# Kernel optimization log

Measured on AMD Instinct MI355X. Metric: run time of the kernel, lower is better.

Reference implementation:

```python
import jax, jax.numpy as jnp
import numpy as np

NODE_CARDS = [119, 5, 12, 12, 10, 6, 6, 2, 2]
EDGE_CARDS = [5, 6, 2]
HIDDEN = 256
LAYERS = 5
N = 60000
E = 180000
G = 2048  # num graphs (fixed num_segments)
BN_EPS = 1e-5

_NODE_OFFS = np.concatenate([[0], np.cumsum(NODE_CARDS[:-1])]).astype(np.int32)
_EDGE_OFFS = np.concatenate([[0], np.cumsum(EDGE_CARDS[:-1])]).astype(np.int32)
_NODE_MAX = np.asarray(NODE_CARDS, np.int32) - 1
_EDGE_MAX = np.asarray(EDGE_CARDS, np.int32) - 1


def _cat_sum(x, table, maxs, offs):
    # x: [N, F] int; table: [sum(cards), H] -> [N, H]
    idx = jnp.clip(x, 0, maxs[None, :]) + offs[None, :]
    return table[idx].sum(axis=1)


def setup_inputs() -> dict:
    key = jax.random.key(0)
    ks = jax.random.split(key, 32)
    w = 0.0625  # ~ xavier for 256

    def nrm(k, shape, s=w):
        return jax.random.normal(k, shape, dtype=jnp.float32) * s

    inp = {
        'x': jax.random.randint(ks[0], (N, len(NODE_CARDS)), 0, 119, dtype=jnp.int32),
        'edge_index': jax.random.randint(ks[1], (2, E), 0, N, dtype=jnp.int32),
        'edge_attr': jax.random.randint(ks[2], (E, len(EDGE_CARDS)), 0, 6, dtype=jnp.int32),
        'batch': jnp.sort(jax.random.randint(ks[3], (N,), 0, G, dtype=jnp.int32)),
        # embeddings
        'node_emb': nrm(ks[4], (int(sum(NODE_CARDS)), HIDDEN), 0.1),
        'edge_emb': nrm(ks[5], (int(sum(EDGE_CARDS)), HIDDEN), 0.1),
        'vn_emb': nrm(ks[6], (1, HIDDEN), 0.1),
        # GINE conv: eps + 2-layer MLP per layer (stacked)
        'eps': jnp.zeros((LAYERS,), jnp.float32),
        'W1': nrm(ks[7], (LAYERS, HIDDEN, HIDDEN)),
        'b1': jnp.zeros((LAYERS, HIDDEN), jnp.float32),
        'W2': nrm(ks[8], (LAYERS, HIDDEN, HIDDEN)),
        'b2': jnp.zeros((LAYERS, HIDDEN), jnp.float32),
        # BatchNorm (eval mode: running stats)
        'bn_gamma': jnp.ones((LAYERS, HIDDEN), jnp.float32),
        'bn_beta': jnp.zeros((LAYERS, HIDDEN), jnp.float32),
        'bn_mean': nrm(ks[9], (LAYERS, HIDDEN), 0.02),
        'bn_var': jnp.ones((LAYERS, HIDDEN), jnp.float32),
        # virtual-node MLP per layer
        'vW1': nrm(ks[10], (LAYERS, HIDDEN, HIDDEN)),
        'vb1': jnp.zeros((LAYERS, HIDDEN), jnp.float32),
        'vW2': nrm(ks[11], (LAYERS, HIDDEN, HIDDEN)),
        'vb2': jnp.zeros((LAYERS, HIDDEN), jnp.float32),
        # head MLP (2 layers: hidden->hidden->1)
        'hW1': nrm(ks[12], (HIDDEN, HIDDEN)),
        'hb1': jnp.zeros((HIDDEN,), jnp.float32),
        'hW2': nrm(ks[13], (HIDDEN, 1)),
        'hb2': jnp.zeros((1,), jnp.float32),
    }
    return inp


def reference(x, edge_index, edge_attr, batch,
              node_emb, edge_emb, vn_emb, eps,
              W1, b1, W2, b2,
              bn_gamma, bn_beta, bn_mean, bn_var,
              vW1, vb1, vW2, vb2,
              hW1, hb1, hW2, hb2):
    node_maxs = jnp.asarray(_NODE_MAX)
    node_offs = jnp.asarray(_NODE_OFFS)
    edge_maxs = jnp.asarray(_EDGE_MAX)
    edge_offs = jnp.asarray(_EDGE_OFFS)

    h = _cat_sum(x, node_emb, node_maxs, node_offs)          # [N, H]
    ea = _cat_sum(edge_attr, edge_emb, edge_maxs, edge_offs)  # [E, H]
    src, dst = edge_index[0], edge_index[1]

    vn = jnp.broadcast_to(vn_emb[0], (G, HIDDEN))  # [G, H]

    def mean_pool(h_):
        s = jax.ops.segment_sum(h_, batch, num_segments=G)
        cnt = jax.ops.segment_sum(jnp.ones((h_.shape[0], 1), h_.dtype), batch, num_segments=G)
        return s / jnp.maximum(cnt, 1.0)

    for l in range(LAYERS):
        h = h + vn[batch]
        # GINEConv: msg = relu(x_src + edge_attr); agg scatter-add onto dst
        msg = jax.nn.relu(h[src] + ea)                        # [E, H]
        agg = jax.ops.segment_sum(msg, dst, num_segments=N)   # [N, H]
        z = (1.0 + eps[l]) * h + agg
        z = jax.nn.relu(z @ W1[l] + b1[l]) @ W2[l] + b2[l]
        # BatchNorm1d (eval, running stats)
        z = (z - bn_mean[l]) * (bn_gamma[l] / jnp.sqrt(bn_var[l] + BN_EPS)) + bn_beta[l]
        h = jax.nn.relu(z)
        # virtual-node update
        g = mean_pool(h)
        vn = vn + (jax.nn.relu(g @ vW1[l] + vb1[l]) @ vW2[l] + vb2[l])

    g = mean_pool(h)                                          # [G, H]
    logits = (jax.nn.relu(g @ hW1 + hb1) @ hW2 + hb2).reshape(-1)  # [G]
    return logits
```

## Files before the change

kernel.cpp:

```cpp
#include <hip/hip_runtime.h>

#define NN 60000
#define NE 180000
#define NG 2048
#define NL 5
#define CAP 32

typedef unsigned short u16;
typedef unsigned int u32;
typedef __bf16 bf16x8 __attribute__((ext_vector_type(8)));
typedef float f32x4 __attribute__((ext_vector_type(4)));

__device__ __forceinline__ u16 f2bf(float f) {
    u32 u = __builtin_bit_cast(u32, f);
    u += 0x7FFFu + ((u >> 16) & 1u);
    return (u16)(u >> 16);
}
__device__ __forceinline__ float bf2f(u16 s) {
    return __builtin_bit_cast(float, (u32)s << 16);
}
__device__ __forceinline__ float bflo(u32 w) {
    return __builtin_bit_cast(float, w << 16);
}
__device__ __forceinline__ float bfhi(u32 w) {
    return __builtin_bit_cast(float, w & 0xFFFF0000u);
}
__device__ __forceinline__ u32 pack2bf(float lo, float hi) {
    return (u32)f2bf(lo) | ((u32)f2bf(hi) << 16);
}
__device__ __forceinline__ void gload_lds16(const void* g, void* l) {
    __builtin_amdgcn_global_load_lds(
        (const __attribute__((address_space(1))) unsigned int*)g,
        (__attribute__((address_space(3))) unsigned int*)l, 16, 0, 0);
}
__device__ __forceinline__ int swz(int row, int col) {
    return (row << 9) + ((((col >> 3) ^ (row & 7))) << 4) + ((col & 7) << 1);
}

__constant__ int NODE_OFF[9]  = {0, 119, 124, 136, 148, 158, 164, 170, 172};
__constant__ int NODE_MAXC[9] = {118, 4, 11, 11, 9, 5, 5, 1, 1};

__global__ __launch_bounds__(256) void k_prep_weights(
    const float* __restrict__ W1, const float* __restrict__ W2,
    const float* __restrict__ vW1, const float* __restrict__ vW2,
    const float* __restrict__ hW1, u16* __restrict__ Wt)
{
    int mat = blockIdx.x >> 8;
    int n = blockIdx.x & 255;
    int k = threadIdx.x;
    const float* src;
    if (mat < 5)       src = W1 + (size_t)mat * 65536;
    else if (mat < 10) src = W2 + (size_t)(mat - 5) * 65536;
    else if (mat < 15) src = vW1 + (size_t)(mat - 10) * 65536;
    else if (mat < 20) src = vW2 + (size_t)(mat - 15) * 65536;
    else               src = hW1;
    Wt[(size_t)mat * 65536 + n * 256 + k] = f2bf(src[k * 256 + n]);
}

__global__ __launch_bounds__(256) void k_misc(
    const float* __restrict__ eemb, const int* __restrict__ batch,
    const float* __restrict__ vn_emb,
    u16* __restrict__ comb, int* __restrict__ starts,
    float* __restrict__ vn, u16* __restrict__ vnbf, float* __restrict__ gsum)
{
    int b = blockIdx.x;
    if (b < 2048) {
        int i = b * 256 + threadIdx.x;
        float v = vn_emb[i & 255];
        vn[i] = v;
        vnbf[i] = f2bf(v);
        gsum[i] = 0.f;
    } else if (b < 2108) {
        int r = b - 2048, c = threadIdx.x;
        int a0 = r / 12, a1 = (r % 12) / 2, a2 = r & 1;
        comb[r * 256 + c] = f2bf(eemb[a0 * 256 + c] + eemb[(5 + a1) * 256 + c] +
                                 eemb[(11 + a2) * 256 + c]);
    } else {
        int g = (b - 2108) * 256 + threadIdx.x;
        if (g > NG) return;
        int lo = 0, hi = NN;
        while (lo < hi) {
            int mid = (lo + hi) >> 1;
            if (batch[mid] < g) lo = mid + 1; else hi = mid;
        }
        starts[g] = lo;
    }
}

__global__ __launch_bounds__(256) void k_embed(const int* __restrict__ x,
                                               const float* __restrict__ node_emb,
                                               u16* __restrict__ hbf,
                                               int* __restrict__ deg)
{
    int i = blockIdx.x * 4 + (threadIdx.x >> 6);
    if (i >= NN) return;
    if ((threadIdx.x & 63) == 0) deg[i] = 0;
    int c = (threadIdx.x & 63) * 4;
    float4 s = make_float4(0.f, 0.f, 0.f, 0.f);
#pragma unroll
    for (int f = 0; f < 9; ++f) {
        int xv = x[i * 9 + f];
        xv = xv < 0 ? 0 : (xv > NODE_MAXC[f] ? NODE_MAXC[f] : xv);
        const float4 t = *(const float4*)&node_emb[(size_t)(NODE_OFF[f] + xv) * 256 + c];
        s.x += t.x; s.y += t.y; s.z += t.z; s.w += t.w;
    }
    ushort4 o;
    o.x = f2bf(s.x); o.y = f2bf(s.y); o.z = f2bf(s.z); o.w = f2bf(s.w);
    *(ushort4*)&hbf[(size_t)i * 256 + c] = o;
}

__global__ __launch_bounds__(256) void k_bucket(
    const int* __restrict__ src, const int* __restrict__ dst,
    const int* __restrict__ eattr, int* __restrict__ deg, u32* __restrict__ slots)
{
    int e = blockIdx.x * 256 + threadIdx.x;
    if (e >= NE) return;
    int a0 = eattr[e * 3 + 0]; a0 = a0 < 0 ? 0 : (a0 > 4 ? 4 : a0);
    int a1 = eattr[e * 3 + 1]; a1 = a1 < 0 ? 0 : (a1 > 5 ? 5 : a1);
    int a2 = eattr[e * 3 + 2]; a2 = a2 < 0 ? 0 : (a2 > 1 ? 1 : a2);
    u32 code = (u32)(a0 * 12 + a1 * 2 + a2);
    int d = dst[e];
    int p = atomicAdd(&deg[d], 1);
    if (p < CAP) slots[(size_t)d * CAP + p] = (u32)src[e] | (code << 17);
}

__global__ __launch_bounds__(256) void k_agg(
    const u16* __restrict__ hbf, const u16* __restrict__ vnbf,
    const int* __restrict__ batch, const u32* __restrict__ slots,
    const int* __restrict__ deg, const u16* __restrict__ comb,
    u16* __restrict__ Abf, const float* __restrict__ epsp)
{
    const int wid = threadIdx.x >> 6, lane = threadIdx.x & 63;
    const int half = lane >> 5, l32 = lane & 31;
    const int d = blockIdx.x * 8 + wid * 2 + half;
    const int c = l32 * 8;
    int nd = deg[d];
    nd = nd > CAP ? CAP : nd;

    const u32* sl = slots + (size_t)d * CAP;
    u32 sv_l = (l32 < nd) ? sl[l32] : 0u;
    int b_l = (l32 < nd) ? batch[sv_l & 0x1FFFFu] : 0;

    float acc[8] = {0.f, 0.f, 0.f, 0.f, 0.f, 0.f, 0.f, 0.f};
    for (int p = 0; p < nd; ++p) {
        int srcl = (lane & 32) | p;
        u32 sv = (u32)__shfl((int)sv_l, srcl);
        int b  = __shfl(b_l, srcl);
        int s  = (int)(sv & 0x1FFFFu);
        int code = (int)(sv >> 17);
        const uint4 hv = *(const uint4*)&hbf[(size_t)s * 256 + c];
        const uint4 vv = *(const uint4*)&vnbf[(size_t)b * 256 + c];
        const uint4 tv = *(const uint4*)&comb[(size_t)code * 256 + c];
        const u32* hw = (const u32*)&hv;
        const u32* vw = (const u32*)&vv;
        const u32* tw = (const u32*)&tv;
#pragma unroll
        for (int e = 0; e < 4; ++e) {
            acc[e * 2 + 0] += fmaxf(bflo(hw[e]) + bflo(vw[e]) + bflo(tw[e]), 0.f);
            acc[e * 2 + 1] += fmaxf(bfhi(hw[e]) + bfhi(vw[e]) + bfhi(tw[e]), 0.f);
        }
    }

    int bd = batch[d];
    float ep = 1.0f + *epsp;
    const uint4 hd = *(const uint4*)&hbf[(size_t)d * 256 + c];
    const uint4 vd = *(const uint4*)&vnbf[(size_t)bd * 256 + c];
    const u32* hw = (const u32*)&hd;
    const u32* vw = (const u32*)&vd;
    uint4 o;
    u32* op = (u32*)&o;
#pragma unroll
    for (int e = 0; e < 4; ++e) {
        float lo = (bflo(hw[e]) + bflo(vw[e])) * ep + acc[e * 2 + 0];
        float hi = (bfhi(hw[e]) + bfhi(vw[e])) * ep + acc[e * 2 + 1];
        op[e] = pack2bf(lo, hi);
    }
    *(uint4*)&Abf[(size_t)d * 256 + c] = o;
}

__global__ __launch_bounds__(512, 2) void k_mlp2(
    const u16* __restrict__ Abf, u16* __restrict__ hnxt,
    const int* __restrict__ batch,
    const u16* __restrict__ W1t, const u16* __restrict__ W2t,
    const float* __restrict__ b1, const float* __restrict__ b2,
    const float* __restrict__ bng, const float* __restrict__ bnb,
    const float* __restrict__ bnm, const float* __restrict__ bnv,
    float* __restrict__ gsum)
{
    __shared__ __align__(16) u16 Tl[128 * 256];
    __shared__ int batchLds[128];
    const int m0 = blockIdx.x * 128;
    const int tid = threadIdx.x, lane = tid & 63, wid = tid >> 6;
    const int wn = wid * 32;
    const int cl = lane & 15, rg = lane >> 4;

    if (tid < 128) batchLds[tid] = (m0 + tid < NN) ? batch[m0 + tid] : -1;

    bf16x8 B1[2][8], B2[2][8];
#pragma unroll
    for (int j = 0; j < 2; ++j) {
        const char* w1p = (const char*)W1t + (size_t)(wn + j * 16 + cl) * 512 + (rg << 4);
        const char* w2p = (const char*)W2t + (size_t)(wn + j * 16 + cl) * 512 + (rg << 4);
#pragma unroll
        for (int ks = 0; ks < 8; ++ks) {
            B1[j][ks] = __builtin_bit_cast(bf16x8, *(const uint4*)(w1p + ks * 64));
            B2[j][ks] = __builtin_bit_cast(bf16x8, *(const uint4*)(w2p + ks * 64));
        }
    }

#pragma unroll
    for (int i = 0; i < 8; ++i) {
        int slot = i * 512 + tid;
        int row = slot >> 5, cch = slot & 31;
        int g = cch ^ (row & 7);
        gload_lds16((const char*)Abf + (size_t)(m0 + row) * 512 + (g << 4),
                    (char*)Tl + ((i * 512 + wid * 64) << 4));
    }
    __syncthreads();

    f32x4 acc[8][2] = {};
#pragma unroll
    for (int ks = 0; ks < 8; ++ks) {
#pragma unroll
        for (int i = 0; i < 8; ++i) {
            int ar = i * 16 + cl;
            int ch = ks * 4 + rg;
            bf16x8 af = __builtin_bit_cast(bf16x8,
                *(const uint4*)((const char*)Tl + (ar << 9) + ((ch ^ (ar & 7)) << 4)));
#pragma unroll
            for (int j = 0; j < 2; ++j)
                acc[i][j] = __builtin_amdgcn_mfma_f32_16x16x32_bf16(af, B1[j][ks], acc[i][j], 0, 0, 0);
        }
    }
    __syncthreads();

#pragma unroll
    for (int j = 0; j < 2; ++j) {
        int col = wn + j * 16 + cl;
        float bv = b1[col];
#pragma unroll
        for (int i = 0; i < 8; ++i)
#pragma unroll
            for (int r = 0; r < 4; ++r) {
                int row = i * 16 + rg * 4 + r;
                float v = fmaxf(acc[i][j][r] + bv, 0.f);
                *(u16*)((char*)Tl + swz(row, col)) = f2bf(v);
            }
    }
    __syncthreads();

#pragma unroll
    for (int i = 0; i < 8; ++i)
#pragma unroll
        for (int j = 0; j < 2; ++j)
            acc[i][j] = f32x4{0.f, 0.f, 0.f, 0.f};
#pragma unroll
    for (int ks = 0; ks < 8; ++ks) {
#pragma unroll
        for (int i = 0; i < 8; ++i) {
            int ar = i * 16 + cl;
            int ch = ks * 4 + rg;
            bf16x8 af = __builtin_bit_cast(bf16x8,
                *(const uint4*)((const char*)Tl + (ar << 9) + ((ch ^ (ar & 7)) << 4)));
#pragma unroll
            for (int j = 0; j < 2; ++j)
                acc[i][j] = __builtin_amdgcn_mfma_f32_16x16x32_bf16(af, B2[j][ks], acc[i][j], 0, 0, 0);
        }
    }

#pragma unroll
    for (int j = 0; j < 2; ++j) {
        int gn = wn + j * 16 + cl;
        float bv = b2[gn];
        float sc = bng[gn] * rsqrtf(bnv[gn] + 1e-5f);
        float sh = bnb[gn] - bnm[gn] * sc;
        float s = 0.f;
        int gcur = -1;
#pragma unroll
        for (int i = 0; i < 8; ++i) {
#pragma unroll
            for (int r = 0; r < 4; ++r) {
                int row = i * 16 + rg * 4 + r;
                int g = batchLds[row];
                float v = acc[i][j][r] + bv;
                u16 hb = f2bf(fmaxf(v * sc + sh, 0.f));
                if (g >= 0) hnxt[(size_t)(m0 + row) * 256 + gn] = hb;
                if (g != gcur) {
                    if (gcur >= 0) atomicAdd(&gsum[(size_t)gcur * 256 + gn], s);
                    gcur = g; s = 0.f;
                }
                if (g >= 0) s += bf2f(hb);
            }
        }
        if (gcur >= 0) atomicAdd(&gsum[(size_t)gcur * 256 + gn], s);
    }
}

__device__ __forceinline__ void stageW(const u16* __restrict__ W, u16* Bl,
                                       int k0, int tid, int wid)
{
#pragma unroll
    for (int i = 0; i < 4; ++i) {
        int slot = i * 512 + tid;
        int row = slot >> 3, cch = slot & 7;
        int g = cch ^ (row & 7);
        gload_lds16((const char*)W + (size_t)row * 512 + (size_t)k0 * 2 + (g << 4),
                    (char*)Bl + ((i * 512 + wid * 64) << 4));
    }
}

__device__ __forceinline__ void gemm64(const u16* Tl, u16* Bl, const u16* __restrict__ W,
                                       f32x4 (&acc)[2][4], int wm, int wn,
                                       int lane, int tid, int wid)
{
    const int cl = lane & 15;
    for (int k0 = 0; k0 < 256; k0 += 64) {
        __syncthreads();
        stageW(W, Bl, k0, tid, wid);
        __syncthreads();
#pragma unroll
        for (int kw = 0; kw < 2; ++kw) {
            int q = kw * 4 + (lane >> 4);
            int qt = (k0 >> 3) + q;
            bf16x8 af[2], bfr[4];
#pragma unroll
            for (int t = 0; t < 2; ++t) {
                int ar = wm + t * 16 + cl;
                af[t] = __builtin_bit_cast(bf16x8,
                    *(const uint4*)((const char*)Tl + (ar << 9) + ((qt ^ (ar & 7)) << 4)));
            }
#pragma unroll
            for (int t = 0; t < 4; ++t) {
                int br = wn + t * 16 + cl;
                bfr[t] = __builtin_bit_cast(bf16x8,
                    *(const uint4*)((const char*)Bl + (br << 7) + ((q ^ (br & 7)) << 4)));
            }
#pragma unroll
            for (int i = 0; i < 2; ++i)
#pragma unroll
                for (int j = 0; j < 4; ++j)
                    acc[i][j] = __builtin_amdgcn_mfma_f32_16x16x32_bf16(af[i], bfr[j], acc[i][j], 0, 0, 0);
        }
    }
}

__device__ __forceinline__ void writeT(u16* Tl, const f32x4 (&acc)[2][4],
                                       const float* __restrict__ b1,
                                       int wm, int wn, int lane)
{
    const int cl = lane & 15, rg = lane >> 4;
#pragma unroll
    for (int j = 0; j < 4; ++j) {
        int col = wn + j * 16 + cl;
        float bv = b1[col];
#pragma unroll
        for (int i = 0; i < 2; ++i)
#pragma unroll
            for (int r = 0; r < 4; ++r) {
                int row = wm + i * 16 + rg * 4 + r;
                float v = fmaxf(acc[i][j][r] + bv, 0.f);
                *(u16*)((char*)Tl + swz(row, col)) = f2bf(v);
            }
    }
}

__global__ __launch_bounds__(512) void k_vnmlp(
    float* __restrict__ gsum, const int* __restrict__ starts,
    const u16* __restrict__ W1t, const u16* __restrict__ W2t,
    const float* __restrict__ b1, const float* __restrict__ b2,
    float* __restrict__ vn, u16* __restrict__ vnbf)
{
    __shared__ __align__(16) u16 Bl[256 * 64];
    __shared__ __align__(16) u16 Tl[64 * 256];
    const int m0 = blockIdx.x * 64;
    const int tid = threadIdx.x, lane = tid & 63, wid = tid >> 6;
    const int wm = (wid >> 2) * 32, wn = (wid & 3) * 64;
    const int cl = lane & 15, rg = lane >> 4;

    {
        const int c = lane * 4;
#pragma unroll
        for (int n = 0; n < 8; ++n) {
            int row = wid * 8 + n;
            int g = m0 + row;
            float4 sv = *(const float4*)&gsum[(size_t)g * 256 + c];
            *(float4*)&gsum[(size_t)g * 256 + c] = make_float4(0.f, 0.f, 0.f, 0.f);
            float cnt = (float)(starts[g + 1] - starts[g]);
            float inv = 1.0f / fmaxf(cnt, 1.0f);
            ushort4 o;
            o.x = f2bf(sv.x * inv); o.y = f2bf(sv.y * inv);
            o.z = f2bf(sv.z * inv); o.w = f2bf(sv.w * inv);
            *(ushort4*)((char*)Tl + swz(row, c)) = o;
        }
    }
    __syncthreads();

    f32x4 acc1[2][4] = {};
    gemm64(Tl, Bl, W1t, acc1, wm, wn, lane, tid, wid);
    __syncthreads();
    writeT(Tl, acc1, b1, wm, wn, lane);

    f32x4 acc2[2][4] = {};
    gemm64(Tl, Bl, W2t, acc2, wm, wn, lane, tid, wid);

#pragma unroll
    for (int j = 0; j < 4; ++j) {
        int gn = wn + j * 16 + cl;
        float bv = b2[gn];
#pragma unroll
        for (int i = 0; i < 2; ++i) {
#pragma unroll
            for (int r = 0; r < 4; ++r) {
                int gm = m0 + wm + i * 16 + rg * 4 + r;
                size_t idx = (size_t)gm * 256 + gn;
                float nv = vn[idx] + acc2[i][j][r] + bv;
                vn[idx] = nv;
                vnbf[idx] = f2bf(nv);
            }
        }
    }
}

__global__ __launch_bounds__(512) void k_headf(
    const float* __restrict__ gsum, const int* __restrict__ starts,
    const u16* __restrict__ W1t, const float* __restrict__ b1,
    const float* __restrict__ hW2, const float* __restrict__ hb2,
    float* __restrict__ out)
{
    __shared__ __align__(16) u16 Bl[256 * 64];
    __shared__ __align__(16) u16 Tl[64 * 256];
    const int m0 = blockIdx.x * 64;
    const int tid = threadIdx.x, lane = tid & 63, wid = tid >> 6;
    const int wm = (wid >> 2) * 32, wn = (wid & 3) * 64;

    {
        const int c = lane * 4;
#pragma unroll
        for (int n = 0; n < 8; ++n) {
            int row = wid * 8 + n;
            int g = m0 + row;
            float4 sv = *(const float4*)&gsum[(size_t)g * 256 + c];
            float cnt = (float)(starts[g + 1] - starts[g]);
            float inv = 1.0f / fmaxf(cnt, 1.0f);
            ushort4 o;
            o.x = f2bf(sv.x * inv); o.y = f2bf(sv.y * inv);
            o.z = f2bf(sv.z * inv); o.w = f2bf(sv.w * inv);
            *(ushort4*)((char*)Tl + swz(row, c)) = o;
        }
    }
    __syncthreads();

    f32x4 acc1[2][4] = {};
    gemm64(Tl, Bl, W1t, acc1, wm, wn, lane, tid, wid);
    __syncthreads();
    writeT(Tl, acc1, b1, wm, wn, lane);
    __syncthreads();

    int row = tid >> 3, oct = tid & 7;
    float s = 0.f;
#pragma unroll
    for (int c = 0; c < 32; ++c) {
        int col = oct * 32 + c;
        s += bf2f(*(const u16*)((const char*)Tl + swz(row, col))) * hW2[col];
    }
    s += __shfl_down(s, 4);
    s += __shfl_down(s, 2);
    s += __shfl_down(s, 1);
    if (oct == 0) out[m0 + row] = s + hb2[0];
}

extern "C" void kernel_launch(void* const* d_in, const int* in_sizes, int n_in,
                              void* d_out, int out_size, void* d_ws, size_t ws_size,
                              hipStream_t stream)
{
    const int*   x        = (const int*)d_in[0];
    const int*   ei       = (const int*)d_in[1];
    const int*   eattr    = (const int*)d_in[2];
    const int*   batch    = (const int*)d_in[3];
    const float* node_emb = (const float*)d_in[4];
    const float* edge_emb = (const float*)d_in[5];
    const float* vn_emb   = (const float*)d_in[6];
    const float* eps      = (const float*)d_in[7];
    const float* W1       = (const float*)d_in[8];
    const float* b1       = (const float*)d_in[9];
    const float* W2       = (const float*)d_in[10];
    const float* b2       = (const float*)d_in[11];
    const float* bng      = (const float*)d_in[12];
    const float* bnb      = (const float*)d_in[13];
    const float* bnm      = (const float*)d_in[14];
    const float* bnv      = (const float*)d_in[15];
    const float* vW1      = (const float*)d_in[16];
    const float* vb1      = (const float*)d_in[17];
    const float* vW2      = (const float*)d_in[18];
    const float* vb2      = (const float*)d_in[19];
    const float* hW1      = (const float*)d_in[20];
    const float* hb1      = (const float*)d_in[21];
    const float* hW2      = (const float*)d_in[22];
    const float* hb2      = (const float*)d_in[23];
    float* out = (float*)d_out;

    char* ws = (char*)d_ws;
    size_t off = 0;
    auto alloc = [&](size_t b) {
        char* p = ws + off;
        off = (off + b + 255) & ~(size_t)255;
        return p;
    };
    u16*   hbf0 = (u16*)alloc((size_t)NN * 256 * 2);
    u16*   hbf1 = (u16*)alloc((size_t)NN * 256 * 2);
    u16*   Abf  = (u16*)alloc((size_t)NN * 256 * 2 + 65536);
    float* vn   = (float*)alloc((size_t)NG * 256 * 4);
    u16*   vnbf = (u16*)alloc((size_t)NG * 256 * 2);
    float* gsum = (float*)alloc((size_t)NG * 256 * 4);
    u16*   Wt   = (u16*)alloc((size_t)21 * 65536 * 2);
    int*   starts = (int*)alloc((size_t)(NG + 1) * 4);
    u16*   comb = (u16*)alloc((size_t)60 * 256 * 2);
    int*   deg  = (int*)alloc((size_t)NN * 4);
    u32*   slots = (u32*)alloc((size_t)NN * CAP * 4);

    const int* srcI = ei;
    const int* dstI = ei + NE;

    k_prep_weights<<<21 * 256, 256, 0, stream>>>(W1, W2, vW1, vW2, hW1, Wt);
    k_misc<<<2117, 256, 0, stream>>>(edge_emb, batch, vn_emb, comb, starts, vn, vnbf, gsum);
    k_embed<<<NN / 4, 256, 0, stream>>>(x, node_emb, hbf0, deg);
    k_bucket<<<(NE + 255) / 256, 256, 0, stream>>>(srcI, dstI, eattr, deg, slots);

    const int GBIG = (NN + 127) / 128;
    const int GSM  = NG / 64;

    u16* hcur = hbf0;
    u16* hnxt = hbf1;
    for (int l = 0; l < NL; ++l) {
        k_agg<<<NN / 8, 256, 0, stream>>>(hcur, vnbf, batch, slots, deg, comb, Abf, eps + l);
        k_mlp2<<<GBIG, 512, 0, stream>>>(Abf, hnxt, batch,
                                         Wt + (size_t)(0 + l) * 65536,
                                         Wt + (size_t)(5 + l) * 65536,
                                         b1 + l * 256, b2 + l * 256,
                                         bng + l * 256, bnb + l * 256,
                                         bnm + l * 256, bnv + l * 256,
                                         gsum);
        if (l < NL - 1) {
            k_vnmlp<<<GSM, 512, 0, stream>>>(gsum, starts,
                                             Wt + (size_t)(10 + l) * 65536,
                                             Wt + (size_t)(15 + l) * 65536,
                                             vb1 + l * 256, vb2 + l * 256,
                                             vn, vnbf);
        }
        u16* t = hcur; hcur = hnxt; hnxt = t;
    }
    k_headf<<<GSM, 512, 0, stream>>>(gsum, starts, Wt + (size_t)20 * 65536,
                                     hb1, hW2, hb2, out);
}
```

Measured before the change: 551.8 us.

## Halve MLP row tile and stream weights in K-halves to raise occupancy

The fused two-layer MLP kernel now handles 64 rows per block instead of 128. Weights are loaded in two K-halves that are reused across register buffers, so the next half's weights load while the current half's MFMAs run. Register and LDS use per block roughly halve, which lets launch bounds request 4 blocks per CU instead of 2 and doubles the grid to fill the GPU better. In exchange each block re-reads all weights for half as many rows, doubling global weight traffic per row. The extra blocks also double the atomic flushes of the per-graph pooled sums.

```diff
diff --git a/kernel.cpp b/kernel.cpp
--- a/kernel.cpp
+++ b/kernel.cpp
@@ -178,7 +178,36 @@
     *(uint4*)&Abf[(size_t)d * 256 + c] = o;
 }
 
-__global__ __launch_bounds__(512, 2) void k_mlp2(
+__device__ __forceinline__ void loadW(bf16x8 (&B)[2][4], const u16* __restrict__ W,
+                                      int hk, int wn, int cl, int rg)
+{
+#pragma unroll
+    for (int j = 0; j < 2; ++j) {
+        const char* p = (const char*)W + (size_t)(wn + j * 16 + cl) * 512 + hk * 256 + (rg << 4);
+#pragma unroll
+        for (int ks = 0; ks < 4; ++ks)
+            B[j][ks] = __builtin_bit_cast(bf16x8, *(const uint4*)(p + ks * 64));
+    }
+}
+
+__device__ __forceinline__ void gemmHalf(f32x4 (&acc)[4][2], const bf16x8 (&B)[2][4],
+                                         const u16* Tl, int hk, int cl, int rg)
+{
+#pragma unroll
+    for (int ks = 0; ks < 4; ++ks) {
+#pragma unroll
+        for (int i = 0; i < 4; ++i) {
+            int ar = i * 16 + cl;
+            int ch = hk * 16 + ks * 4 + rg;
+            bf16x8 af = __builtin_bit_cast(bf16x8,
+                *(const uint4*)((const char*)Tl + (ar << 9) + ((ch ^ (ar & 7)) << 4)));
+            acc[i][0] = __builtin_amdgcn_mfma_f32_16x16x32_bf16(af, B[0][ks], acc[i][0], 0, 0, 0);
+            acc[i][1] = __builtin_amdgcn_mfma_f32_16x16x32_bf16(af, B[1][ks], acc[i][1], 0, 0, 0);
+        }
+    }
+}
+
+__global__ __launch_bounds__(512, 4) void k_mlp3(
     const u16* __restrict__ Abf, u16* __restrict__ hnxt,
     const int* __restrict__ batch,
     const u16* __restrict__ W1t, const u16* __restrict__ W2t,
@@ -187,51 +216,35 @@
     const float* __restrict__ bnm, const float* __restrict__ bnv,
     float* __restrict__ gsum)
 {
-    __shared__ __align__(16) u16 Tl[128 * 256];
-    __shared__ int batchLds[128];
-    const int m0 = blockIdx.x * 128;
+    __shared__ __align__(16) u16 Tl[64 * 256];
+    __shared__ int batchLds[64];
+    const int m0 = blockIdx.x * 64;
     const int tid = threadIdx.x, lane = tid & 63, wid = tid >> 6;
     const int wn = wid * 32;
     const int cl = lane & 15, rg = lane >> 4;
 
-    if (tid < 128) batchLds[tid] = (m0 + tid < NN) ? batch[m0 + tid] : -1;
-
-    bf16x8 B1[2][8], B2[2][8];
-#pragma unroll
-    for (int j = 0; j < 2; ++j) {
-        const char* w1p = (const char*)W1t + (size_t)(wn + j * 16 + cl) * 512 + (rg << 4);
-        const char* w2p = (const char*)W2t + (size_t)(wn + j * 16 + cl) * 512 + (rg << 4);
-#pragma unroll
-        for (int ks = 0; ks < 8; ++ks) {
-            B1[j][ks] = __builtin_bit_cast(bf16x8, *(const uint4*)(w1p + ks * 64));
-            B2[j][ks] = __builtin_bit_cast(bf16x8, *(const uint4*)(w2p + ks * 64));
-        }
-    }
-
-#pragma unroll
-    for (int i = 0; i < 8; ++i) {
+    if (tid < 64) batchLds[tid] = (m0 + tid < NN) ? batch[m0 + tid] : -1;
+
+    bf16x8 Ba[2][4], Bb[2][4];
+    loadW(Ba, W1t, 0, wn, cl, rg);
+
+#pragma unroll
+    for (int i = 0; i < 4; ++i) {
         int slot = i * 512 + tid;
         int row = slot >> 5, cch = slot & 31;
         int g = cch ^ (row & 7);
         gload_lds16((const char*)Abf + (size_t)(m0 + row) * 512 + (g << 4),
                     (char*)Tl + ((i * 512 + wid * 64) << 4));
     }
-    __syncthreads();
-
-    f32x4 acc[8][2] = {};
-#pragma unroll
-    for (int ks = 0; ks < 8; ++ks) {
-#pragma unroll
-        for (int i = 0; i < 8; ++i) {
-            int ar = i * 16 + cl;
-            int ch = ks * 4 + rg;
-            bf16x8 af = __builtin_bit_cast(bf16x8,
-                *(const uint4*)((const char*)Tl + (ar << 9) + ((ch ^ (ar & 7)) << 4)));
-#pragma unroll
-            for (int j = 0; j < 2; ++j)
-                acc[i][j] = __builtin_amdgcn_mfma_f32_16x16x32_bf16(af, B1[j][ks], acc[i][j], 0, 0, 0);
-        }
-    }
+    loadW(Bb, W1t, 1, wn, cl, rg);
+
+    __syncthreads();
+
+    f32x4 acc1[4][2] = {};
+    gemmHalf(acc1, Ba, Tl, 0, cl, rg);
+    loadW(Ba, W2t, 0, wn, cl, rg);
+    gemmHalf(acc1, Bb, Tl, 1, cl, rg);
+    loadW(Bb, W2t, 1, wn, cl, rg);
     __syncthreads();
 
 #pragma unroll
@@ -239,34 +252,19 @@
         int col = wn + j * 16 + cl;
         float bv = b1[col];
 #pragma unroll
-        for (int i = 0; i < 8; ++i)
+        for (int i = 0; i < 4; ++i)
 #pragma unroll
             for (int r = 0; r < 4; ++r) {
                 int row = i * 16 + rg * 4 + r;
-                float v = fmaxf(acc[i][j][r] + bv, 0.f);
+                float v = fmaxf(acc1[i][j][r] + bv, 0.f);
                 *(u16*)((char*)Tl + swz(row, col)) = f2bf(v);
             }
     }
     __syncthreads();
 
-#pragma unroll
-    for (int i = 0; i < 8; ++i)
-#pragma unroll
-        for (int j = 0; j < 2; ++j)
-            acc[i][j] = f32x4{0.f, 0.f, 0.f, 0.f};
-#pragma unroll
-    for (int ks = 0; ks < 8; ++ks) {
-#pragma unroll
-        for (int i = 0; i < 8; ++i) {
-            int ar = i * 16 + cl;
-            int ch = ks * 4 + rg;
-            bf16x8 af = __builtin_bit_cast(bf16x8,
-                *(const uint4*)((const char*)Tl + (ar << 9) + ((ch ^ (ar & 7)) << 4)));
-#pragma unroll
-            for (int j = 0; j < 2; ++j)
-                acc[i][j] = __builtin_amdgcn_mfma_f32_16x16x32_bf16(af, B2[j][ks], acc[i][j], 0, 0, 0);
-        }
-    }
+    f32x4 acc2[4][2] = {};
+    gemmHalf(acc2, Ba, Tl, 0, cl, rg);
+    gemmHalf(acc2, Bb, Tl, 1, cl, rg);
 
 #pragma unroll
     for (int j = 0; j < 2; ++j) {
@@ -277,12 +275,12 @@
         float s = 0.f;
         int gcur = -1;
 #pragma unroll
-        for (int i = 0; i < 8; ++i) {
+        for (int i = 0; i < 4; ++i) {
 #pragma unroll
             for (int r = 0; r < 4; ++r) {
                 int row = i * 16 + rg * 4 + r;
                 int g = batchLds[row];
-                float v = acc[i][j][r] + bv;
+                float v = acc2[i][j][r] + bv;
                 u16 hb = f2bf(fmaxf(v * sc + sh, 0.f));
                 if (g >= 0) hnxt[(size_t)(m0 + row) * 256 + gn] = hb;
                 if (g != gcur) {
@@ -526,14 +524,14 @@
     k_embed<<<NN / 4, 256, 0, stream>>>(x, node_emb, hbf0, deg);
     k_bucket<<<(NE + 255) / 256, 256, 0, stream>>>(srcI, dstI, eattr, deg, slots);
 
-    const int GBIG = (NN + 127) / 128;
+    const int GBIG = (NN + 63) / 64;
     const int GSM  = NG / 64;
 
     u16* hcur = hbf0;
     u16* hnxt = hbf1;
     for (int l = 0; l < NL; ++l) {
         k_agg<<<NN / 8, 256, 0, stream>>>(hcur, vnbf, batch, slots, deg, comb, Abf, eps + l);
-        k_mlp2<<<GBIG, 512, 0, stream>>>(Abf, hnxt, batch,
+        k_mlp3<<<GBIG, 512, 0, stream>>>(Abf, hnxt, batch,
                                          Wt + (size_t)(0 + l) * 65536,
                                          Wt + (size_t)(5 + l) * 65536,
                                          b1 + l * 256, b2 + l * 256,
```

New measurement: 545.5 us. Within noise of the previous version (-1.1%).
